# Kernel tuning notes

Hardware: AMD Instinct MI355X
Metric: run time of the kernel (lower is better)

The kernel has to match this reference:

```python
import jax, jax.numpy as jnp
import numpy as np

B, T, N, F_IN = 8, 288, 2000, 1
E, ID, H, K = 128, 16, 128, 20
FL = T // 2 + 1  # rfft length = in_len//2 + 1
EPS_NORM = 1e-12
EPS_LN = 1e-8


def setup_inputs() -> dict:
    key = jax.random.key(0)
    k0, k1, k2, k3, k4 = jax.random.split(key, 5)
    return {
        "x": jax.random.normal(k0, (B, T, N, F_IN), jnp.float32),
        "Ex": jax.random.normal(k1, (FL, E), jnp.float32),
        "nodes": jax.random.normal(k2, (N, ID), jnp.float32),
        "Wd": jax.random.normal(k3, (N, E + ID, H), jnp.float32),
        "Wxabs": jax.random.normal(k4, (H, H), jnp.float32),
    }


def reference(x, Ex, nodes, Wd, Wxabs):
    # [B,T,N,F] -> take feature 0 -> [B,N,T]
    xt = jnp.transpose(x[:, :, :, 0], (0, 2, 1))
    xf = jnp.abs(jnp.fft.rfft(xt, axis=-1))  # [B,N,FL]
    # F.normalize p=2 over dim=1 (nodes), then dim=2 (freq): x / max(||x||, eps)
    xf = xf / jnp.clip(jnp.sqrt(jnp.sum(xf * xf, axis=1, keepdims=True)), EPS_NORM)
    xf = xf / jnp.clip(jnp.sqrt(jnp.sum(xf * xf, axis=2, keepdims=True)), EPS_NORM)
    xe = jnp.matmul(xf, Ex)  # [B,N,E]
    # cat(): append static node identity embedding per batch element
    xk = jnp.concatenate(
        [xe, jnp.broadcast_to(nodes, (xe.shape[0], N, ID))], axis=-1
    )  # [B,N,E+ID]
    # per-node weight bmm: [N,B,E+ID] @ [N,E+ID,H] -> [B,N,H]
    x1 = jax.nn.relu(jnp.einsum('bnd,ndh->bnh', xk, Wd))
    # LayerNorm over last two dims [N,H], eps=1e-8, no affine
    mu = jnp.mean(x1, axis=(1, 2), keepdims=True)
    var = jnp.mean((x1 - mu) ** 2, axis=(1, 2), keepdims=True)
    x2 = (x1 - mu) / jnp.sqrt(var + EPS_LN)
    # dropout is identity at inference
    adp = jnp.einsum('bnh,hk->bnk', x2, Wxabs)  # convt
    adj = jnp.einsum('bnh,bmh->bnm', adp, x1)  # [B,N,N]
    adp = jax.nn.relu(adj)
    # dy_mask_graph: per-row topk over dim=2 (torch dim=1 of the [N,N] slice),
    # binary mask via scatter of ones, then elementwise mask
    _, idx = jax.lax.top_k(adp, K)  # [B,N,K]
    bi = jnp.arange(adp.shape[0])[:, None, None]
    ni = jnp.arange(N)[None, :, None]
    mask = jnp.zeros_like(adp).at[bi, ni, idx].set(1.0)
    adj_masked = adp * mask
    return jax.nn.softmax(adj_masked, axis=2)
```

## Files before the change

### kernel.cpp

```cpp
#include <hip/hip_runtime.h>
#include <math.h>

#define BB 8
#define TT 288
#define NN 2000
#define FLEN 145
#define EE 128
#define IDD 16
#define HH 128
#define DKK 144
#define KTOP 20

typedef _Float16 half8 __attribute__((ext_vector_type(8)));
typedef float f32x4 __attribute__((ext_vector_type(4)));
typedef unsigned short ushort_t;

#define OFF_TW  ((size_t)0)
#define SZ_TW   ((size_t)TT*FLEN*2)
#define OFF_XF  (OFF_TW + SZ_TW)
#define SZ_XF   ((size_t)BB*FLEN*NN)
#define OFF_ICN (OFF_XF + SZ_XF)
#define OFF_IRN (OFF_ICN + (size_t)BB*FLEN)
#define OFF_XE  (OFF_IRN + (size_t)BB*NN)
#define SZ_BNH  ((size_t)BB*NN*HH)
#define OFF_X1  (OFF_XE + SZ_BNH)
#define OFF_ADP (OFF_X1 + SZ_BNH)
#define OFF_CSW (OFF_ADP + SZ_BNH)
#define OFF_LNS (OFF_CSW + HH)
#define OFF_LNF (OFF_LNS + 16)

#define CACHE_W 2064
#define FUSED_LDS_BYTES ((16 * CACHE_W + 2 * 16 * 64) * 4)

__device__ __forceinline__ float wredSum(float v) {
#pragma unroll
  for (int o = 32; o > 0; o >>= 1) v += __shfl_down(v, o, 64);
  return v;
}
__device__ __forceinline__ float wredMax(float v) {
#pragma unroll
  for (int o = 32; o > 0; o >>= 1) v = fmaxf(v, __shfl_down(v, o, 64));
  return v;
}
__device__ __forceinline__ float wredSumAll(float v) {
#pragma unroll
  for (int o = 32; o > 0; o >>= 1) v += __shfl_xor(v, o, 64);
  return v;
}
__device__ __forceinline__ float wredMaxAll(float v) {
#pragma unroll
  for (int o = 32; o > 0; o >>= 1) v = fmaxf(v, __shfl_xor(v, o, 64));
  return v;
}

__device__ __forceinline__ void split16(float v, ushort_t& hi, ushort_t& lo) {
  _Float16 h = (_Float16)v;
  _Float16 l = (_Float16)(v - (float)h);
  union { _Float16 f; ushort_t u; } a, b;
  a.f = h; b.f = l;
  hi = a.u; lo = b.u;
}

__global__ void k_init(const float* __restrict__ Wx, float* __restrict__ csw,
                       float* __restrict__ lns) {
  int k = threadIdx.x;
  float s = 0.f;
  for (int h = 0; h < HH; ++h) s += Wx[h * HH + k];
  csw[k] = s;
  if (k < 16) lns[k] = 0.f;
}

__global__ void k_tw(float* __restrict__ tw) {
  int id = blockIdx.x * 256 + threadIdx.x;
  if (id >= TT * FLEN) return;
  int t = id / FLEN, f = id % FLEN;
  int r = (t * f) % TT;
  double th = -2.0 * 3.14159265358979323846 * (double)r / (double)TT;
  tw[2 * id]     = (float)cos(th);
  tw[2 * id + 1] = (float)sin(th);
}

__global__ void k_dft(const float* __restrict__ x, const float* __restrict__ tw,
                      float* __restrict__ xf) {
  __shared__ __align__(16) float Xs[16][128];
  __shared__ __align__(16) float TWs[16][32][2];
  const int b = blockIdx.z;
  const int f0 = blockIdx.y * 32;
  const int n0 = blockIdx.x * 128;
  const int tid = threadIdx.x;
  const int tn = tid & 31;
  const int tf = tid >> 5;
  float ar[4][4] = {}, ai[4][4] = {};
  for (int t0 = 0; t0 < TT; t0 += 16) {
    __syncthreads();
    for (int l = tid; l < 512; l += 256) {
      int row = l >> 5, q = l & 31;
      int n = n0 + q * 4;
      const float* src = x + ((size_t)b * TT + (t0 + row)) * NN + n;
      float4 v = make_float4(0, 0, 0, 0);
      if (n + 3 < NN) v = *(const float4*)src;
      else {
        if (n + 0 < NN) v.x = src[0];
        if (n + 1 < NN) v.y = src[1];
        if (n + 2 < NN) v.z = src[2];
        if (n + 3 < NN) v.w = src[3];
      }
      *(float4*)&Xs[row][q * 4] = v;
    }
    for (int l = tid; l < 512; l += 256) {
      int row = l >> 5, ff = l & 31;
      int f = f0 + ff;
      float2 cs = make_float2(0, 0);
      if (f < FLEN) cs = *(const float2*)&tw[((size_t)(t0 + row) * FLEN + f) * 2];
      *(float2*)&TWs[row][ff][0] = cs;
    }
    __syncthreads();
#pragma unroll 4
    for (int t = 0; t < 16; ++t) {
      float4 xv = *(float4*)&Xs[t][tn * 4];
      float xx[4] = {xv.x, xv.y, xv.z, xv.w};
      float4 p0 = *(float4*)&TWs[t][tf * 4][0];
      float4 p1 = *(float4*)&TWs[t][tf * 4 + 2][0];
      float c[4] = {p0.x, p0.z, p1.x, p1.z};
      float s[4] = {p0.y, p0.w, p1.y, p1.w};
#pragma unroll
      for (int i = 0; i < 4; ++i)
#pragma unroll
        for (int j = 0; j < 4; ++j) {
          ar[i][j] = fmaf(xx[j], c[i], ar[i][j]);
          ai[i][j] = fmaf(xx[j], s[i], ai[i][j]);
        }
    }
  }
#pragma unroll
  for (int i = 0; i < 4; ++i) {
    int f = f0 + tf * 4 + i;
    if (f >= FLEN) continue;
    float* dst = &xf[((size_t)b * FLEN + f) * NN];
    float o[4];
#pragma unroll
    for (int j = 0; j < 4; ++j)
      o[j] = sqrtf(ar[i][j] * ar[i][j] + ai[i][j] * ai[i][j]);
    int n = n0 + tn * 4;
    if (n + 3 < NN) *(float4*)&dst[n] = make_float4(o[0], o[1], o[2], o[3]);
    else {
#pragma unroll
      for (int j = 0; j < 4; ++j) if (n + j < NN) dst[n + j] = o[j];
    }
  }
}

__global__ void k_colnorm(const float* __restrict__ xf, float* __restrict__ icn) {
  __shared__ float sc[4];
  int bf = blockIdx.x;
  const float* rowp = xf + (size_t)bf * NN;
  float s = 0.f;
  for (int i = threadIdx.x; i < NN; i += 256) { float v = rowp[i]; s = fmaf(v, v, s); }
  s = wredSum(s);
  int lane = threadIdx.x & 63, w = threadIdx.x >> 6;
  if (lane == 0) sc[w] = s;
  __syncthreads();
  if (threadIdx.x == 0)
    icn[bf] = 1.f / fmaxf(sqrtf(sc[0] + sc[1] + sc[2] + sc[3]), 1e-12f);
}

__global__ void k_rownorm(const float* __restrict__ xf, const float* __restrict__ icn,
                          float* __restrict__ irn) {
  int b = blockIdx.y;
  int n = blockIdx.x * 256 + threadIdx.x;
  if (n >= NN) return;
  float s = 0.f;
  for (int f = 0; f < FLEN; ++f) {
    float v = xf[((size_t)b * FLEN + f) * NN + n] * icn[b * FLEN + f];
    s = fmaf(v, v, s);
  }
  irn[b * NN + n] = 1.f / fmaxf(sqrtf(s), 1e-12f);
}

__global__ void k_xe(const float* __restrict__ xf, const float* __restrict__ icn,
                     const float* __restrict__ irn, const float* __restrict__ Ex,
                     float* __restrict__ xe) {
  __shared__ __align__(16) float As[16][64];
  __shared__ __align__(16) float Bs[16][128];
  const int b = blockIdx.y;
  const int n0 = blockIdx.x * 64;
  const int tid = threadIdx.x;
  const int tn = tid >> 4, te = tid & 15;
  float acc[4][8] = {};
  for (int f0 = 0; f0 < 160; f0 += 16) {
    __syncthreads();
    {
      int kt = tid >> 4, q = tid & 15;
      int f = f0 + kt;
      int n = n0 + q * 4;
      float4 v = make_float4(0, 0, 0, 0);
      if (f < FLEN) {
        float ic = icn[b * FLEN + f];
        const float* src = &xf[((size_t)b * FLEN + f) * NN + n];
        if (n + 3 < NN) v = *(const float4*)src;
        else {
          if (n + 0 < NN) v.x = src[0];
          if (n + 1 < NN) v.y = src[1];
          if (n + 2 < NN) v.z = src[2];
          if (n + 3 < NN) v.w = src[3];
        }
        v.x *= ic; v.y *= ic; v.z *= ic; v.w *= ic;
      }
      *(float4*)&As[kt][q * 4] = v;
    }
    for (int l = tid; l < 512; l += 256) {
      int kt = l >> 5, q = l & 31;
      int f = f0 + kt;
      float4 v = make_float4(0, 0, 0, 0);
      if (f < FLEN) v = *(const float4*)&Ex[(size_t)f * EE + q * 4];
      *(float4*)&Bs[kt][q * 4] = v;
    }
    __syncthreads();
#pragma unroll
    for (int k = 0; k < 16; ++k) {
      float4 a  = *(float4*)&As[k][tn * 4];
      float4 b0 = *(float4*)&Bs[k][te * 4];
      float4 b1 = *(float4*)&Bs[k][64 + te * 4];
      float av[4] = {a.x, a.y, a.z, a.w};
      float bv[8] = {b0.x, b0.y, b0.z, b0.w, b1.x, b1.y, b1.z, b1.w};
#pragma unroll
      for (int i = 0; i < 4; ++i)
#pragma unroll
        for (int j = 0; j < 8; ++j)
          acc[i][j] = fmaf(av[i], bv[j], acc[i][j]);
    }
  }
#pragma unroll
  for (int i = 0; i < 4; ++i) {
    int n = n0 + tn * 4 + i;
    if (n >= NN) continue;
    float sc = irn[b * NN + n];
    float* dst = &xe[((size_t)b * NN + n) * EE];
    *(float4*)&dst[te * 4] =
        make_float4(acc[i][0] * sc, acc[i][1] * sc, acc[i][2] * sc, acc[i][3] * sc);
    *(float4*)&dst[64 + te * 4] =
        make_float4(acc[i][4] * sc, acc[i][5] * sc, acc[i][6] * sc, acc[i][7] * sc);
  }
}

__global__ void k_x1(const float* xe, const float* __restrict__ nodes,
                     const float* __restrict__ Wd, float* __restrict__ x1,
                     ushort_t* x1hl) {
  __shared__ __align__(16) float xk[8][DKK];
  __shared__ float red[4][32][33];
  const int n = blockIdx.x;
  const int tid = threadIdx.x;
  {
    int b = tid >> 5, q = tid & 31;
    *(float4*)&xk[b][q * 4] = *(const float4*)&xe[((size_t)b * NN + n) * EE + q * 4];
  }
  if (tid < 128) {
    int b = tid >> 4, i = tid & 15;
    xk[b][EE + i] = nodes[(size_t)n * IDD + i];
  }
  __syncthreads();
  const int h4 = tid & 31;
  const int dg = tid >> 5;
  float acc[8][4] = {};
  for (int d = dg; d < DKK; d += 8) {
    float4 wv = *(const float4*)&Wd[((size_t)n * DKK + d) * HH + h4 * 4];
#pragma unroll
    for (int b = 0; b < 8; ++b) {
      float xv = xk[b][d];
      acc[b][0] = fmaf(xv, wv.x, acc[b][0]);
      acc[b][1] = fmaf(xv, wv.y, acc[b][1]);
      acc[b][2] = fmaf(xv, wv.z, acc[b][2]);
      acc[b][3] = fmaf(xv, wv.w, acc[b][3]);
    }
  }
#pragma unroll
  for (int b = 0; b < 8; ++b)
#pragma unroll
    for (int j = 0; j < 4; ++j)
      acc[b][j] += __shfl_xor(acc[b][j], 32, 64);
  const int wv_ = tid >> 6, lane = tid & 63;
  if (lane < 32) {
#pragma unroll
    for (int b = 0; b < 8; ++b)
#pragma unroll
      for (int j = 0; j < 4; ++j)
        red[wv_][lane][b * 4 + j] = acc[b][j];
  }
  __syncthreads();
#pragma unroll
  for (int o = 0; o < 4; ++o) {
    int idx = tid + o * 256;
    int b = idx >> 7, h = idx & 127;
    float s = red[0][h >> 2][b * 4 + (h & 3)] + red[1][h >> 2][b * 4 + (h & 3)] +
              red[2][h >> 2][b * 4 + (h & 3)] + red[3][h >> 2][b * 4 + (h & 3)];
    s = fmaxf(s, 0.f);
    x1[((size_t)b * NN + n) * HH + h] = s;
    ushort_t hi, lo;
    split16(s, hi, lo);
    size_t base = ((size_t)b * NN + n) * 256;
    x1hl[base + h] = hi;
    x1hl[base + 128 + h] = lo;
  }
}

__global__ void k_ln_stats(const float* __restrict__ x1, float* __restrict__ lns) {
  __shared__ float sc[4], sc2[4];
  int b = blockIdx.y, chunk = blockIdx.x;
  const float* base = x1 + (size_t)b * NN * HH + (size_t)chunk * 8000;
  float s = 0.f, s2 = 0.f;
  for (int i = threadIdx.x; i < 8000; i += 256) {
    float v = base[i];
    s += v; s2 = fmaf(v, v, s2);
  }
  s = wredSum(s); s2 = wredSum(s2);
  int lane = threadIdx.x & 63, w = threadIdx.x >> 6;
  if (lane == 0) { sc[w] = s; sc2[w] = s2; }
  __syncthreads();
  if (threadIdx.x == 0) {
    atomicAdd(&lns[b], sc[0] + sc[1] + sc[2] + sc[3]);
    atomicAdd(&lns[8 + b], sc2[0] + sc2[1] + sc2[2] + sc2[3]);
  }
}

__global__ void k_ln_final(const float* __restrict__ lns, float* __restrict__ lnf) {
  int b = threadIdx.x;
  if (b < 8) {
    float cnt = (float)(NN * HH);
    float mu = lns[b] / cnt;
    float var = fmaxf(lns[8 + b] / cnt - mu * mu, 0.f);
    lnf[b] = mu;
    lnf[8 + b] = 1.f / sqrtf(var + 1e-8f);
  }
}

__global__ void k_adp(const float* __restrict__ x1, const float* __restrict__ Wx,
                      const float* __restrict__ csw, const float* __restrict__ lnf,
                      ushort_t* __restrict__ adphl) {
  __shared__ __align__(16) float As[16][64];
  __shared__ __align__(16) float Bs[16][128];
  const int r0 = blockIdx.x * 64;
  const int tid = threadIdx.x;
  const int tn = tid >> 4, te = tid & 15;
  float acc[4][8] = {};
  for (int k0 = 0; k0 < HH; k0 += 16) {
    __syncthreads();
    {
      int rr = tid >> 2, kq = tid & 3;
      float4 v = *(const float4*)&x1[(size_t)(r0 + rr) * HH + k0 + kq * 4];
      As[kq * 4 + 0][rr] = v.x;
      As[kq * 4 + 1][rr] = v.y;
      As[kq * 4 + 2][rr] = v.z;
      As[kq * 4 + 3][rr] = v.w;
    }
    for (int l = tid; l < 512; l += 256) {
      int kt = l >> 5, q = l & 31;
      *(float4*)&Bs[kt][q * 4] = *(const float4*)&Wx[(size_t)(k0 + kt) * HH + q * 4];
    }
    __syncthreads();
#pragma unroll
    for (int k = 0; k < 16; ++k) {
      float4 a  = *(float4*)&As[k][tn * 4];
      float4 b0 = *(float4*)&Bs[k][te * 4];
      float4 b1 = *(float4*)&Bs[k][64 + te * 4];
      float av[4] = {a.x, a.y, a.z, a.w};
      float bv[8] = {b0.x, b0.y, b0.z, b0.w, b1.x, b1.y, b1.z, b1.w};
#pragma unroll
      for (int i = 0; i < 4; ++i)
#pragma unroll
        for (int j = 0; j < 8; ++j)
          acc[i][j] = fmaf(av[i], bv[j], acc[i][j]);
    }
  }
  float4 c0 = *(const float4*)&csw[te * 4];
  float4 c1 = *(const float4*)&csw[64 + te * 4];
  float cw[8] = {c0.x, c0.y, c0.z, c0.w, c1.x, c1.y, c1.z, c1.w};
#pragma unroll
  for (int i = 0; i < 4; ++i) {
    int r = r0 + tn * 4 + i;
    int b = r / NN;
    float mu = lnf[b], isd = lnf[8 + b];
    size_t base = (size_t)r * 256;
    ushort_t hi[8], lo[8];
#pragma unroll
    for (int j = 0; j < 8; ++j) {
      float o = (acc[i][j] - mu * cw[j]) * isd;
      split16(o, hi[j], lo[j]);
    }
    ushort4 u;
    u.x = hi[0]; u.y = hi[1]; u.z = hi[2]; u.w = hi[3];
    *(ushort4*)&adphl[base + te * 4] = u;
    u.x = hi[4]; u.y = hi[5]; u.z = hi[6]; u.w = hi[7];
    *(ushort4*)&adphl[base + 64 + te * 4] = u;
    u.x = lo[0]; u.y = lo[1]; u.z = lo[2]; u.w = lo[3];
    *(ushort4*)&adphl[base + 128 + te * 4] = u;
    u.x = lo[4]; u.y = lo[5]; u.z = lo[6]; u.w = lo[7];
    *(ushort4*)&adphl[base + 128 + 64 + te * 4] = u;
  }
}

__global__ __launch_bounds__(1024, 1) void k_fused(
    const ushort_t* __restrict__ adphl, const ushort_t* __restrict__ x1hl,
    float* __restrict__ out) {
  extern __shared__ float smem[];
  float* cache = smem;
  float* scrV = smem + 16 * CACHE_W;
  int*   scrI = (int*)(scrV + 16 * 64);

  const int b = blockIdx.y;
  const int n0 = blockIdx.x * 16;
  const int tid = threadIdx.x;
  const int w = tid >> 6;
  const int lane = tid & 63;
  const int quad = lane >> 4, r16 = lane & 15;

  half8 Ah[4], Al[4];
  {
    const ushort_t* abase =
        adphl + ((size_t)(b * NN + n0 + r16)) * 256 + quad * 8;
#pragma unroll
    for (int ks = 0; ks < 4; ++ks) {
      Ah[ks] = *(const half8*)(abase + ks * 32);
      Al[ks] = *(const half8*)(abase + 128 + ks * 32);
    }
  }
  const int mbase = w * 128;

  half8 Bh0[4], Bl0[4], Bh1[4], Bl1[4];

#define LOADB(I, BH, BL)                                                      \
  {                                                                           \
    int mt_ = mbase + (I) * 16 + r16;                                         \
    int mc_ = (mt_ < NN) ? mt_ : NN - 1;                                      \
    const ushort_t* bb_ = x1hl + ((size_t)(b * NN + mc_)) * 256 + quad * 8;   \
    BH[0] = *(const half8*)(bb_);       BL[0] = *(const half8*)(bb_ + 128);   \
    BH[1] = *(const half8*)(bb_ + 32);  BL[1] = *(const half8*)(bb_ + 160);   \
    BH[2] = *(const half8*)(bb_ + 64);  BL[2] = *(const half8*)(bb_ + 192);   \
    BH[3] = *(const half8*)(bb_ + 96);  BL[3] = *(const half8*)(bb_ + 224);   \
  }

#define STEP(I, BH, BL, BH2, BL2)                                             \
  {                                                                           \
    if ((I) < 7) LOADB((I) + 1, BH2, BL2);                                    \
    f32x4 acc = (f32x4){0.f, 0.f, 0.f, 0.f};                                  \
    _Pragma("unroll")                                                         \
    for (int ks = 0; ks < 4; ++ks) {                                          \
      acc = __builtin_amdgcn_mfma_f32_16x16x32_f16(Ah[ks], BH[ks], acc, 0, 0, 0); \
      acc = __builtin_amdgcn_mfma_f32_16x16x32_f16(Ah[ks], BL[ks], acc, 0, 0, 0); \
      acc = __builtin_amdgcn_mfma_f32_16x16x32_f16(Al[ks], BH[ks], acc, 0, 0, 0); \
    }                                                                         \
    int mt_ = mbase + (I) * 16 + r16;                                         \
    _Pragma("unroll")                                                         \
    for (int reg = 0; reg < 4; ++reg) {                                       \
      int row_ = quad * 4 + reg;                                              \
      float v_ = (mt_ < NN) ? fmaxf(acc[reg], 0.f) : -1.f;                    \
      cache[row_ * CACHE_W + mt_] = v_;                                       \
    }                                                                         \
  }

  LOADB(0, Bh0, Bl0);
  STEP(0, Bh0, Bl0, Bh1, Bl1);
  STEP(1, Bh1, Bl1, Bh0, Bl0);
  STEP(2, Bh0, Bl0, Bh1, Bl1);
  STEP(3, Bh1, Bl1, Bh0, Bl0);
  STEP(4, Bh0, Bl0, Bh1, Bl1);
  STEP(5, Bh1, Bl1, Bh0, Bl0);
  STEP(6, Bh0, Bl0, Bh1, Bl1);
  STEP(7, Bh1, Bl1, Bh0, Bl0);
#undef STEP
#undef LOADB

  __syncthreads();

  {
    const int row = w;
    const float* crow = cache + row * CACHE_W;
    f32x4 V[8];
#pragma unroll
    for (int j = 0; j < 8; ++j)
      V[j] = *(const f32x4*)&crow[j * 256 + lane * 4];

    float mx = -1.f, cp = 0.f;
#pragma unroll
    for (int j = 0; j < 8; ++j)
#pragma unroll
      for (int e = 0; e < 4; ++e) {
        mx = fmaxf(mx, V[j][e]);
        cp += (V[j][e] > 0.f) ? 1.f : 0.f;
      }
    const float m = wredMaxAll(mx);
    const float cpos = wredSumAll(cp);
    const float em = expf(-m);
    float* g = out + ((size_t)(b * NN + n0 + row)) * NN;

    if (cpos <= 20.5f) {
      float s = 0.f;
#pragma unroll
      for (int j = 0; j < 8; ++j)
#pragma unroll
        for (int e = 0; e < 4; ++e)
          if (V[j][e] > 0.f) s += expf(V[j][e] - m);
      s = wredSumAll(s);
      const float invD = 1.f / (s + (2000.f - cpos) * em);
      const float defv = em * invD;
#pragma unroll
      for (int j = 0; j < 8; ++j) {
        int m0 = j * 256 + lane * 4;
        if (m0 >= NN) continue;
        float4 o;
        o.x = (V[j][0] > 0.f) ? expf(V[j][0] - m) * invD : defv;
        o.y = (V[j][1] > 0.f) ? expf(V[j][1] - m) * invD : defv;
        o.z = (V[j][2] > 0.f) ? expf(V[j][2] - m) * invD : defv;
        o.w = (V[j][3] > 0.f) ? expf(V[j][3] - m) * invD : defv;
        *(float4*)&g[m0] = o;
      }
    } else {
      float tval = 0.f, cf = cpos;
      if (cpos > 64.5f) {
        float tlo = 0.f, thi = m;
        bool found = false;
        for (int it = 0; it < 64 && !found; ++it) {
          float mid = (it < 12)
              ? 0.5f * (tlo + thi)
              : __uint_as_float((__float_as_uint(tlo) + __float_as_uint(thi)) >> 1);
          float c = 0.f;
#pragma unroll
          for (int j = 0; j < 8; ++j)
#pragma unroll
            for (int e = 0; e < 4; ++e)
              c += (V[j][e] > mid) ? 1.f : 0.f;
          c = wredSumAll(c);
          if (c > 64.5f) tlo = mid;
          else if (c < 19.5f) thi = mid;
          else { tval = mid; cf = c; found = true; }
        }
        if (!found) { tval = tlo; cf = 64.f; }
      }
      int cI = (int)(cf + 0.5f);
      if (cI > 64) cI = 64;

      float* sv = scrV + w * 64;
      int* si = scrI + w * 64;
      int base = 0;
#pragma unroll
      for (int j = 0; j < 8; ++j)
#pragma unroll
        for (int e = 0; e < 4; ++e) {
          bool p = V[j][e] > tval;
          unsigned long long msk = __ballot(p);
          if (p) {
            int pos = base + (int)__popcll(msk & ((1ull << lane) - 1ull));
            if (pos < 64) { sv[pos] = V[j][e]; si[pos] = j * 256 + lane * 4 + e; }
          }
          base += (int)__popcll(msk);
        }
      asm volatile("s_waitcnt lgkmcnt(0)" ::: "memory");

      float cv = (lane < cI) ? sv[lane] : -1.f;
      int ci = (lane < cI) ? si[lane] : 0x7fffffff;
#pragma unroll
      for (int k = 2; k <= 64; k <<= 1)
#pragma unroll
        for (int j = k >> 1; j > 0; j >>= 1) {
          float ov = __shfl_xor(cv, j, 64);
          int oi = __shfl_xor(ci, j, 64);
          bool otherBetter = (ov > cv) || (ov == cv && oi < ci);
          bool iAmLow = (lane & j) == 0;
          bool desc = (lane & k) == 0;
          bool take = (desc == iAmLow) ? otherBetter : !otherBetter;
          if (take) { cv = ov; ci = oi; }
        }
      const float t20 = __shfl(cv, 19, 64);
      float e20 = (lane < 20) ? expf(cv - m) : 0.f;
      const float s20 = wredSumAll(e20);
      const float invD = 1.f / (s20 + (2000.f - 20.f) * em);
      const float defv = em * invD;
#pragma unroll
      for (int j = 0; j < 8; ++j) {
        int m0 = j * 256 + lane * 4;
        if (m0 >= NN) continue;
        float4 o;
        o.x = (V[j][0] >= t20) ? expf(V[j][0] - m) * invD : defv;
        o.y = (V[j][1] >= t20) ? expf(V[j][1] - m) * invD : defv;
        o.z = (V[j][2] >= t20) ? expf(V[j][2] - m) * invD : defv;
        o.w = (V[j][3] >= t20) ? expf(V[j][3] - m) * invD : defv;
        *(float4*)&g[m0] = o;
      }
    }
  }
}

extern "C" void kernel_launch(void* const* d_in, const int* in_sizes, int n_in,
                              void* d_out, int out_size, void* d_ws, size_t ws_size,
                              hipStream_t stream) {
  const float* x     = (const float*)d_in[0];
  const float* Ex    = (const float*)d_in[1];
  const float* nodes = (const float*)d_in[2];
  const float* Wd    = (const float*)d_in[3];
  const float* Wx    = (const float*)d_in[4];
  float* out = (float*)d_out;
  float* w = (float*)d_ws;
  float* tw  = w + OFF_TW;
  float* xf  = w + OFF_XF;
  float* icn = w + OFF_ICN;
  float* irn = w + OFF_IRN;
  float* xe  = w + OFF_XE;
  float* x1  = w + OFF_X1;
  float* csw = w + OFF_CSW;
  float* lns = w + OFF_LNS;
  float* lnf = w + OFF_LNF;
  ushort_t* adphl = (ushort_t*)(w + OFF_ADP);
  ushort_t* x1hl  = (ushort_t*)(w + OFF_XE);

  static int _once = []() {
    (void)hipFuncSetAttribute((const void*)k_fused,
                              hipFuncAttributeMaxDynamicSharedMemorySize,
                              FUSED_LDS_BYTES);
    return 0;
  }();
  (void)_once;

  k_init<<<1, 128, 0, stream>>>(Wx, csw, lns);
  k_tw<<<(TT * FLEN + 255) / 256, 256, 0, stream>>>(tw);
  k_dft<<<dim3(16, 5, BB), 256, 0, stream>>>(x, tw, xf);
  k_colnorm<<<BB * FLEN, 256, 0, stream>>>(xf, icn);
  k_rownorm<<<dim3(8, BB), 256, 0, stream>>>(xf, icn, irn);
  k_xe<<<dim3(32, BB), 256, 0, stream>>>(xf, icn, irn, Ex, xe);
  k_x1<<<NN, 256, 0, stream>>>(xe, nodes, Wd, x1, x1hl);
  k_ln_stats<<<dim3(32, BB), 256, 0, stream>>>(x1, lns);
  k_ln_final<<<1, 64, 0, stream>>>(lns, lnf);
  k_adp<<<250, 256, 0, stream>>>(x1, Wx, csw, lnf, adphl);
  k_fused<<<dim3(125, BB), 1024, FUSED_LDS_BYTES, stream>>>(adphl, x1hl, out);
}
```

Measured before the change: 571.5 us.

## Split fused adjacency GEMM and top-k softmax into two kernels via global memory

Replaces the single LDS-heavy fused kernel, one 1024-thread block per CU, with two kernels. The first computes relu(adp·x1ᵀ) with MFMA in 256-thread blocks and writes it directly to the output buffer. The second re-reads each row, performs top-20 masking and softmax, and overwrites it in place. This removes the large LDS footprint and the block-wide barrier to raise occupancy and parallelism. The cost is an extra full round trip of the B×N×N tensor through global memory.

```diff
diff --git a/kernel.cpp b/kernel.cpp
--- a/kernel.cpp
+++ b/kernel.cpp
@@ -28,9 +28,6 @@
 #define OFF_CSW (OFF_ADP + SZ_BNH)
 #define OFF_LNS (OFF_CSW + HH)
 #define OFF_LNF (OFF_LNS + 16)
-
-#define CACHE_W 2064
-#define FUSED_LDS_BYTES ((16 * CACHE_W + 2 * 16 * 64) * 4)
 
 __device__ __forceinline__ float wredSum(float v) {
 #pragma unroll
@@ -398,16 +395,11 @@
   }
 }
 
-__global__ __launch_bounds__(1024, 1) void k_fused(
+__global__ __launch_bounds__(256, 2) void k_adjT(
     const ushort_t* __restrict__ adphl, const ushort_t* __restrict__ x1hl,
     float* __restrict__ out) {
-  extern __shared__ float smem[];
-  float* cache = smem;
-  float* scrV = smem + 16 * CACHE_W;
-  int*   scrI = (int*)(scrV + 16 * 64);
-
-  const int b = blockIdx.y;
-  const int n0 = blockIdx.x * 16;
+  const int b = blockIdx.z;
+  const int n0 = blockIdx.y * 16;
   const int tid = threadIdx.x;
   const int w = tid >> 6;
   const int lane = tid & 63;
@@ -423,7 +415,8 @@
       Al[ks] = *(const half8*)(abase + 128 + ks * 32);
     }
   }
-  const int mbase = w * 128;
+  const int mbase = blockIdx.x * 512 + w * 128;
+  float* obase = out + ((size_t)(b * NN + n0 + quad * 4)) * NN;
 
   half8 Bh0[4], Bl0[4], Bh1[4], Bl1[4];
 
@@ -449,11 +442,10 @@
       acc = __builtin_amdgcn_mfma_f32_16x16x32_f16(Al[ks], BH[ks], acc, 0, 0, 0); \
     }                                                                         \
     int mt_ = mbase + (I) * 16 + r16;                                         \
-    _Pragma("unroll")                                                         \
-    for (int reg = 0; reg < 4; ++reg) {                                       \
-      int row_ = quad * 4 + reg;                                              \
-      float v_ = (mt_ < NN) ? fmaxf(acc[reg], 0.f) : -1.f;                    \
-      cache[row_ * CACHE_W + mt_] = v_;                                       \
+    if (mt_ < NN) {                                                           \
+      _Pragma("unroll")                                                       \
+      for (int reg = 0; reg < 4; ++reg)                                       \
+        obase[(size_t)reg * NN + mt_] = fmaxf(acc[reg], 0.f);                 \
     }                                                                         \
   }
 
@@ -468,123 +460,128 @@
   STEP(7, Bh1, Bl1, Bh0, Bl0);
 #undef STEP
 #undef LOADB
-
-  __syncthreads();
-
-  {
-    const int row = w;
-    const float* crow = cache + row * CACHE_W;
-    f32x4 V[8];
+}
+
+__global__ __launch_bounds__(256, 4) void k_topsm(float* out) {
+  __shared__ float scrV[4][64];
+  __shared__ int scrI[4][64];
+  const int tid = threadIdx.x;
+  const int w = tid >> 6, lane = tid & 63;
+  const int r = blockIdx.x * 4 + w;
+  float* g = out + (size_t)r * NN;
+
+  f32x4 V[8];
+#pragma unroll
+  for (int j = 0; j < 8; ++j) {
+    int m0 = j * 256 + lane * 4;
+    if (m0 < NN) V[j] = *(const f32x4*)&g[m0];
+    else V[j] = (f32x4){-1.f, -1.f, -1.f, -1.f};
+  }
+
+  float mx = -1.f, cp = 0.f;
+#pragma unroll
+  for (int j = 0; j < 8; ++j)
+#pragma unroll
+    for (int e = 0; e < 4; ++e) {
+      mx = fmaxf(mx, V[j][e]);
+      cp += (V[j][e] > 0.f) ? 1.f : 0.f;
+    }
+  const float m = wredMaxAll(mx);
+  const float cpos = wredSumAll(cp);
+  const float em = expf(-m);
+
+  if (cpos <= 20.5f) {
+    float s = 0.f;
 #pragma unroll
     for (int j = 0; j < 8; ++j)
-      V[j] = *(const f32x4*)&crow[j * 256 + lane * 4];
-
-    float mx = -1.f, cp = 0.f;
+#pragma unroll
+      for (int e = 0; e < 4; ++e)
+        if (V[j][e] > 0.f) s += expf(V[j][e] - m);
+    s = wredSumAll(s);
+    const float invD = 1.f / (s + (2000.f - cpos) * em);
+    const float defv = em * invD;
+#pragma unroll
+    for (int j = 0; j < 8; ++j) {
+      int m0 = j * 256 + lane * 4;
+      if (m0 >= NN) continue;
+      float4 o;
+      o.x = (V[j][0] > 0.f) ? expf(V[j][0] - m) * invD : defv;
+      o.y = (V[j][1] > 0.f) ? expf(V[j][1] - m) * invD : defv;
+      o.z = (V[j][2] > 0.f) ? expf(V[j][2] - m) * invD : defv;
+      o.w = (V[j][3] > 0.f) ? expf(V[j][3] - m) * invD : defv;
+      *(float4*)&g[m0] = o;
+    }
+  } else {
+    float tval = 0.f, cf = cpos;
+    if (cpos > 64.5f) {
+      float tlo = 0.f, thi = m;
+      bool found = false;
+      for (int it = 0; it < 64 && !found; ++it) {
+        float mid = (it < 12)
+            ? 0.5f * (tlo + thi)
+            : __uint_as_float((__float_as_uint(tlo) + __float_as_uint(thi)) >> 1);
+        float c = 0.f;
+#pragma unroll
+        for (int j = 0; j < 8; ++j)
+#pragma unroll
+          for (int e = 0; e < 4; ++e)
+            c += (V[j][e] > mid) ? 1.f : 0.f;
+        c = wredSumAll(c);
+        if (c > 64.5f) tlo = mid;
+        else if (c < 19.5f) thi = mid;
+        else { tval = mid; cf = c; found = true; }
+      }
+      if (!found) { tval = tlo; cf = 64.f; }
+    }
+    int cI = (int)(cf + 0.5f);
+    if (cI > 64) cI = 64;
+
+    float* sv = scrV[w];
+    int* si = scrI[w];
+    int base = 0;
 #pragma unroll
     for (int j = 0; j < 8; ++j)
 #pragma unroll
       for (int e = 0; e < 4; ++e) {
-        mx = fmaxf(mx, V[j][e]);
-        cp += (V[j][e] > 0.f) ? 1.f : 0.f;
+        bool p = V[j][e] > tval;
+        unsigned long long msk = __ballot(p);
+        if (p) {
+          int pos = base + (int)__popcll(msk & ((1ull << lane) - 1ull));
+          if (pos < 64) { sv[pos] = V[j][e]; si[pos] = j * 256 + lane * 4 + e; }
+        }
+        base += (int)__popcll(msk);
       }
-    const float m = wredMaxAll(mx);
-    const float cpos = wredSumAll(cp);
-    const float em = expf(-m);
-    float* g = out + ((size_t)(b * NN + n0 + row)) * NN;
-
-    if (cpos <= 20.5f) {
-      float s = 0.f;
-#pragma unroll
-      for (int j = 0; j < 8; ++j)
-#pragma unroll
-        for (int e = 0; e < 4; ++e)
-          if (V[j][e] > 0.f) s += expf(V[j][e] - m);
-      s = wredSumAll(s);
-      const float invD = 1.f / (s + (2000.f - cpos) * em);
-      const float defv = em * invD;
-#pragma unroll
-      for (int j = 0; j < 8; ++j) {
-        int m0 = j * 256 + lane * 4;
-        if (m0 >= NN) continue;
-        float4 o;
-        o.x = (V[j][0] > 0.f) ? expf(V[j][0] - m) * invD : defv;
-        o.y = (V[j][1] > 0.f) ? expf(V[j][1] - m) * invD : defv;
-        o.z = (V[j][2] > 0.f) ? expf(V[j][2] - m) * invD : defv;
-        o.w = (V[j][3] > 0.f) ? expf(V[j][3] - m) * invD : defv;
-        *(float4*)&g[m0] = o;
+    asm volatile("s_waitcnt lgkmcnt(0)" ::: "memory");
+
+    float cv = (lane < cI) ? sv[lane] : -1.f;
+    int ci = (lane < cI) ? si[lane] : 0x7fffffff;
+#pragma unroll
+    for (int k = 2; k <= 64; k <<= 1)
+#pragma unroll
+      for (int j = k >> 1; j > 0; j >>= 1) {
+        float ov = __shfl_xor(cv, j, 64);
+        int oi = __shfl_xor(ci, j, 64);
+        bool otherBetter = (ov > cv) || (ov == cv && oi < ci);
+        bool iAmLow = (lane & j) == 0;
+        bool desc = (lane & k) == 0;
+        bool take = (desc == iAmLow) ? otherBetter : !otherBetter;
+        if (take) { cv = ov; ci = oi; }
       }
-    } else {
-      float tval = 0.f, cf = cpos;
-      if (cpos > 64.5f) {
-        float tlo = 0.f, thi = m;
-        bool found = false;
-        for (int it = 0; it < 64 && !found; ++it) {
-          float mid = (it < 12)
-              ? 0.5f * (tlo + thi)
-              : __uint_as_float((__float_as_uint(tlo) + __float_as_uint(thi)) >> 1);
-          float c = 0.f;
-#pragma unroll
-          for (int j = 0; j < 8; ++j)
-#pragma unroll
-            for (int e = 0; e < 4; ++e)
-              c += (V[j][e] > mid) ? 1.f : 0.f;
-          c = wredSumAll(c);
-          if (c > 64.5f) tlo = mid;
-          else if (c < 19.5f) thi = mid;
-          else { tval = mid; cf = c; found = true; }
-        }
-        if (!found) { tval = tlo; cf = 64.f; }
-      }
-      int cI = (int)(cf + 0.5f);
-      if (cI > 64) cI = 64;
-
-      float* sv = scrV + w * 64;
-      int* si = scrI + w * 64;
-      int base = 0;
-#pragma unroll
-      for (int j = 0; j < 8; ++j)
-#pragma unroll
-        for (int e = 0; e < 4; ++e) {
-          bool p = V[j][e] > tval;
-          unsigned long long msk = __ballot(p);
-          if (p) {
-            int pos = base + (int)__popcll(msk & ((1ull << lane) - 1ull));
-            if (pos < 64) { sv[pos] = V[j][e]; si[pos] = j * 256 + lane * 4 + e; }
-          }
-          base += (int)__popcll(msk);
-        }
-      asm volatile("s_waitcnt lgkmcnt(0)" ::: "memory");
-
-      float cv = (lane < cI) ? sv[lane] : -1.f;
-      int ci = (lane < cI) ? si[lane] : 0x7fffffff;
-#pragma unroll
-      for (int k = 2; k <= 64; k <<= 1)
-#pragma unroll
-        for (int j = k >> 1; j > 0; j >>= 1) {
-          float ov = __shfl_xor(cv, j, 64);
-          int oi = __shfl_xor(ci, j, 64);
-          bool otherBetter = (ov > cv) || (ov == cv && oi < ci);
-          bool iAmLow = (lane & j) == 0;
-          bool desc = (lane & k) == 0;
-          bool take = (desc == iAmLow) ? otherBetter : !otherBetter;
-          if (take) { cv = ov; ci = oi; }
-        }
-      const float t20 = __shfl(cv, 19, 64);
-      float e20 = (lane < 20) ? expf(cv - m) : 0.f;
-      const float s20 = wredSumAll(e20);
-      const float invD = 1.f / (s20 + (2000.f - 20.f) * em);
-      const float defv = em * invD;
-#pragma unroll
-      for (int j = 0; j < 8; ++j) {
-        int m0 = j * 256 + lane * 4;
-        if (m0 >= NN) continue;
-        float4 o;
-        o.x = (V[j][0] >= t20) ? expf(V[j][0] - m) * invD : defv;
-        o.y = (V[j][1] >= t20) ? expf(V[j][1] - m) * invD : defv;
-        o.z = (V[j][2] >= t20) ? expf(V[j][2] - m) * invD : defv;
-        o.w = (V[j][3] >= t20) ? expf(V[j][3] - m) * invD : defv;
-        *(float4*)&g[m0] = o;
-      }
+    const float t20 = __shfl(cv, 19, 64);
+    float e20 = (lane < 20) ? expf(cv - m) : 0.f;
+    const float s20 = wredSumAll(e20);
+    const float invD = 1.f / (s20 + (2000.f - 20.f) * em);
+    const float defv = em * invD;
+#pragma unroll
+    for (int j = 0; j < 8; ++j) {
+      int m0 = j * 256 + lane * 4;
+      if (m0 >= NN) continue;
+      float4 o;
+      o.x = (V[j][0] >= t20) ? expf(V[j][0] - m) * invD : defv;
+      o.y = (V[j][1] >= t20) ? expf(V[j][1] - m) * invD : defv;
+      o.z = (V[j][2] >= t20) ? expf(V[j][2] - m) * invD : defv;
+      o.w = (V[j][3] >= t20) ? expf(V[j][3] - m) * invD : defv;
+      *(float4*)&g[m0] = o;
     }
   }
 }
@@ -611,14 +608,6 @@
   ushort_t* adphl = (ushort_t*)(w + OFF_ADP);
   ushort_t* x1hl  = (ushort_t*)(w + OFF_XE);
 
-  static int _once = []() {
-    (void)hipFuncSetAttribute((const void*)k_fused,
-                              hipFuncAttributeMaxDynamicSharedMemorySize,
-                              FUSED_LDS_BYTES);
-    return 0;
-  }();
-  (void)_once;
-
   k_init<<<1, 128, 0, stream>>>(Wx, csw, lns);
   k_tw<<<(TT * FLEN + 255) / 256, 256, 0, stream>>>(tw);
   k_dft<<<dim3(16, 5, BB), 256, 0, stream>>>(x, tw, xf);
@@ -629,5 +618,6 @@
   k_ln_stats<<<dim3(32, BB), 256, 0, stream>>>(x1, lns);
   k_ln_final<<<1, 64, 0, stream>>>(lns, lnf);
   k_adp<<<250, 256, 0, stream>>>(x1, Wx, csw, lnf, adphl);
-  k_fused<<<dim3(125, BB), 1024, FUSED_LDS_BYTES, stream>>>(adphl, x1hl, out);
-}
+  k_adjT<<<dim3(4, 125, BB), 256, 0, stream>>>(adphl, x1hl, out);
+  k_topsm<<<(BB * NN) / 4, 256, 0, stream>>>(out);
+}
```

New measurement: 571.2 us. Within noise of the previous version (-0.0%).
